# Kernel tuning notes

Measured on AMD Instinct MI355X. Metric: run time of the kernel, lower is better.

The kernel has to match this reference:

```python
import jax, jax.numpy as jnp
import numpy as np

B, C_IN, C_OUT, RED, H, W = 8, 256, 64, 16, 256, 256
K = 3


def setup_inputs() -> dict:
    key = jax.random.key(0)
    k1, k2, k3, k4, k5 = jax.random.split(key, 5)
    x = jax.random.normal(k1, (B, C_OUT, H, W), dtype=jnp.float32)
    vec = jax.random.normal(k2, (B, C_IN), dtype=jnp.float32)
    # ChanNorm affine params
    g = jnp.ones((1, C_OUT, 1, 1), dtype=jnp.float32)
    b = jnp.zeros((1, C_OUT, 1, 1), dtype=jnp.float32)
    # conv_du MLP (torch Linear weights: [out, in], no bias)
    w1 = jax.random.normal(k3, (C_IN // RED, C_IN), dtype=jnp.float32) / np.sqrt(C_IN)
    w2 = jax.random.normal(k4, (C_OUT, C_IN // RED), dtype=jnp.float32) / np.sqrt(C_IN // RED)
    # Conv2DMod weight, kaiming normal fan_in (leaky_relu a=0): std=sqrt(2/fan_in)
    fan_in = C_OUT * K * K
    wconv = jax.random.normal(k5, (C_OUT, C_OUT, K, K), dtype=jnp.float32) * np.sqrt(2.0 / fan_in)
    return {"x": x, "vec": vec, "g": g, "b": b, "w1": w1, "w2": w2, "wconv": wconv}


def reference(x, vec, g, b, w1, w2, wconv):
    eps_norm = 1e-5
    eps_mod = 1e-8
    # ChanNorm: normalize over channel dim (unbiased=False var)
    mean = jnp.mean(x, axis=1, keepdims=True)
    var = jnp.mean((x - mean) ** 2, axis=1, keepdims=True)
    nx = (x - mean) / jnp.sqrt(var + eps_norm) * g + b
    # style MLP: Linear -> LeakyReLU(0.1) -> Linear (no biases)
    hid = jax.nn.leaky_relu(vec @ w1.T, negative_slope=0.1)
    sty = hid @ w2.T  # [B, C_OUT]
    # per-sample modulated weights: [B, O, I, K, K]
    weights = wconv[None, :, :, :, :] * (sty[:, None, :, None, None] + 1.0)
    # demodulate
    d = jax.lax.rsqrt(jnp.sum(weights ** 2, axis=(2, 3, 4), keepdims=True) + eps_mod)
    weights = weights * d
    # grouped conv with groups=B == per-sample conv; same padding for k=3,s=1,d=1 -> 1
    pad = ((H - 1) * 0 + 1 * (K - 1)) // 2
    def per_sample_conv(xi, wi):
        # xi: [C,H,W], wi: [O,I,K,K]
        return jax.lax.conv_general_dilated(
            xi[None], wi, window_strides=(1, 1),
            padding=[(pad, pad), (pad, pad)],
            dimension_numbers=("NCHW", "OIHW", "NCHW"))[0]
    out = jax.vmap(per_sample_conv)(nx, weights)  # [B, O, H, W]
    return out + x
```

## Files before the change

### kernel.cpp

```cpp
#include <hip/hip_runtime.h>
#include <hip/hip_bf16.h>

typedef __hip_bfloat16 bf16;
typedef __attribute__((ext_vector_type(8))) short short8;
typedef __attribute__((ext_vector_type(4))) float float4v;

#define Hd 256
#define Wd 256
#define HW 65536
#define CO 64

__global__ __launch_bounds__(64) void k1_style(
    const float* __restrict__ vec, const float* __restrict__ w1,
    const float* __restrict__ w2, const float* __restrict__ wconv,
    bf16* __restrict__ wA)
{
    int o = blockIdx.x;
    int s = blockIdx.y;
    int i = threadIdx.x;

    float sv[4];
#pragma unroll
    for (int q = 0; q < 4; ++q) sv[q] = vec[s * 256 + q * 64 + i];

    float hid[16];
#pragma unroll
    for (int j = 0; j < 16; ++j) {
        float p = 0.f;
#pragma unroll
        for (int q = 0; q < 4; ++q) p += sv[q] * w1[j * 256 + q * 64 + i];
#pragma unroll
        for (int off = 32; off >= 1; off >>= 1) p += __shfl_xor(p, off, 64);
        hid[j] = p > 0.f ? p : 0.1f * p;
    }
    float sty = 0.f;
#pragma unroll
    for (int j = 0; j < 16; ++j) sty += w2[i * 16 + j] * hid[j];
    float msty = sty + 1.0f;

    float wrow[9];
#pragma unroll
    for (int tt = 0; tt < 9; ++tt) wrow[tt] = wconv[(o * 64 + i) * 9 + tt] * msty;
    float ss = 0.f;
#pragma unroll
    for (int tt = 0; tt < 9; ++tt) ss += wrow[tt] * wrow[tt];
#pragma unroll
    for (int off = 32; off >= 1; off >>= 1) ss += __shfl_xor(ss, off, 64);
    float d = rsqrtf(ss + 1e-8f);

    bf16* wAs = wA + s * (18 * 64 * 32);
#pragma unroll
    for (int tt = 0; tt < 9; ++tt) {
        int k = tt * 64 + i;
        wAs[(k >> 5) * 2048 + o * 32 + (k & 31)] = (bf16)(wrow[tt] * d);
    }
}

__global__ __launch_bounds__(256) void k2_norm(
    const float* __restrict__ x, const float* __restrict__ gg,
    const float* __restrict__ bb, bf16* __restrict__ nx,
    float2* __restrict__ sms)
{
    int bx  = blockIdx.x;
    int h   = bx >> 1;
    int seg = (bx & 1) * 128;
    int s   = blockIdx.y;
    int t   = threadIdx.x;
    int wave = t >> 6, lane = t & 63;
    int po = lane & 7;
    int cg = lane >> 3;

    __shared__ __align__(16) char lbuf[4][4096];

    int pxw = seg + wave * 32;
    const float* xrow = x + (size_t)s * ((size_t)CO * HW) + (size_t)h * Wd;

    float4 v[8];
#pragma unroll
    for (int c = 0; c < 8; ++c)
        v[c] = *(const float4*)&xrow[(size_t)(cg * 8 + c) * HW + pxw + po * 4];

    float s1[4], s2[4];
#pragma unroll
    for (int pi = 0; pi < 4; ++pi) {
        float a = 0.f, q = 0.f;
#pragma unroll
        for (int c = 0; c < 8; ++c) { float f = (&v[c].x)[pi]; a += f; q += f * f; }
        s1[pi] = a; s2[pi] = q;
    }
#pragma unroll
    for (int off = 8; off <= 32; off <<= 1)
#pragma unroll
        for (int pi = 0; pi < 4; ++pi) {
            s1[pi] += __shfl_xor(s1[pi], off, 64);
            s2[pi] += __shfl_xor(s2[pi], off, 64);
        }
    float mean[4], rstd[4];
#pragma unroll
    for (int pi = 0; pi < 4; ++pi) {
        mean[pi] = s1[pi] * (1.f / 64);
        float var = s2[pi] * (1.f / 64) - mean[pi] * mean[pi] + 1e-5f;
        rstd[pi] = rsqrtf(var);
    }
    if (cg == 0) {
        float2* smsrow = sms + (size_t)s * HW + (size_t)h * Wd;
#pragma unroll
        for (int pi = 0; pi < 4; ++pi) {
            float var = s2[pi] * (1.f / 64) - mean[pi] * mean[pi] + 1e-5f;
            smsrow[pxw + po * 4 + pi] = make_float2(mean[pi], var * rstd[pi]);
        }
    }

    float4 gA = *(const float4*)&gg[cg * 8], gB = *(const float4*)&gg[cg * 8 + 4];
    float4 bA = *(const float4*)&bb[cg * 8], bB = *(const float4*)&bb[cg * 8 + 4];
#pragma unroll
    for (int pi = 0; pi < 4; ++pi) {
        union { uint4 u; bf16 hh[8]; } ov;
#pragma unroll
        for (int c = 0; c < 8; ++c) {
            float gv = (c < 4) ? (&gA.x)[c] : (&gB.x)[c - 4];
            float bv = (c < 4) ? (&bA.x)[c] : (&bB.x)[c - 4];
            ov.hh[c] = (bf16)(((&v[c].x)[pi] - mean[pi]) * rstd[pi] * gv + bv);
        }
        int p = po * 4 + pi;
        *(uint4*)&lbuf[wave][(size_t)p * 128 + cg * 16] = ov.u;
    }
    __syncthreads();
    bf16* nxw = nx + ((size_t)s * HW + (size_t)h * Wd + pxw) * CO;
#pragma unroll
    for (int i = 0; i < 4; ++i) {
        uint4 d = *(uint4*)&lbuf[wave][i * 1024 + lane * 16];
        *(uint4*)((char*)nxw + i * 1024 + lane * 16) = d;
    }
}

#define PXB 32
#define ROWS 8
#define TR 10
#define WL 34
#define NSITES (TR * WL)
#define ROW_ELEMS (8 * WL * 8)

union U4 { uint4 u; bf16 h[8]; short8 s8; };

__global__ __launch_bounds__(256) void k3_conv(
    const bf16* __restrict__ nx, const float2* __restrict__ sms,
    const float* __restrict__ gg, const float* __restrict__ bb,
    const bf16* __restrict__ wA, float* __restrict__ out)
{
    int w0 = blockIdx.x * PXB;
    int h0 = blockIdx.y * ROWS;
    int s  = blockIdx.z;
    int t  = threadIdx.x;
    __shared__ __align__(16) bf16 tile[TR * ROW_ELEMS];
    __shared__ float2 sbi[64];
    if (t < 64) sbi[t] = make_float2(bb[t], 1.0f / gg[t]);

    int p0 = t, p1 = t + 256;
    bool live1 = (p1 < NSITES);
    int dr0 = p0 / WL, wl0 = p0 - dr0 * WL;
    int dr1 = live1 ? (p1 / WL) : 0;
    int wl1 = live1 ? (p1 - dr1 * WL) : 0;
    int grow0 = h0 + dr0 - 1, wab0 = w0 + wl0 - 1;
    int grow1 = h0 + dr1 - 1, wab1 = w0 + wl1 - 1;
    bool ok0 = (grow0 >= 0 && grow0 < Hd && wab0 >= 0 && wab0 < Wd);
    bool ok1 = live1 && (grow1 >= 0 && grow1 < Hd && wab1 >= 0 && wab1 < Wd);
    const bf16* np0 = nx + ((size_t)s * HW + (size_t)grow0 * Wd + wab0) * CO;
    const bf16* np1 = nx + ((size_t)s * HW + (size_t)grow1 * Wd + wab1) * CO;
    bf16* dst0 = &tile[dr0 * ROW_ELEMS + wl0 * 8];
    bf16* dst1 = &tile[dr1 * ROW_ELEMS + wl1 * 8];
    uint4 z = make_uint4(0u, 0u, 0u, 0u);
#pragma unroll
    for (int c8 = 0; c8 < 8; ++c8) {
        uint4 a = ok0 ? *(const uint4*)&np0[c8 * 8] : z;
        *(uint4*)&dst0[c8 * (WL * 8)] = a;
    }
    if (live1) {
#pragma unroll
        for (int c8 = 0; c8 < 8; ++c8) {
            uint4 a = ok1 ? *(const uint4*)&np1[c8 * 8] : z;
            *(uint4*)&dst1[c8 * (WL * 8)] = a;
        }
    }

    int wave = t >> 6, lane = t & 63;
    int mi = wave & 1, ni = wave >> 1;
    int col = lane & 15, quad = lane >> 4;

    const bf16* wAs = wA + s * (18 * 64 * 32);
    const bf16* pa0 = wAs + (mi * 32 + col) * 32 + quad * 8;
    const bf16* pa1 = wAs + (mi * 32 + 16 + col) * 32 + quad * 8;
    U4 a0c, a1c;
    a0c.u = *(const uint4*)pa0;
    a1c.u = *(const uint4*)pa1;

    int wpx = w0 + ni * 16 + col;
    float2 msr[ROWS];
#pragma unroll
    for (int r = 0; r < ROWS; ++r)
        msr[r] = sms[(size_t)s * HW + (size_t)(h0 + r) * Wd + wpx];

    __syncthreads();

    float2 bi8[2][4];
#pragma unroll
    for (int mt = 0; mt < 2; ++mt)
#pragma unroll
        for (int rr = 0; rr < 4; ++rr)
            bi8[mt][rr] = sbi[mi * 32 + mt * 16 + quad * 4 + rr];

    float4v acc[2][ROWS];
#pragma unroll
    for (int mt = 0; mt < 2; ++mt)
#pragma unroll
        for (int r = 0; r < ROWS; ++r) acc[mt][r] = (float4v)0.f;

    int base = ni * 16 + col;
#pragma unroll 1
    for (int kc = 0; kc < 18; ++kc) {
        U4 a0n, a1n;
        a0n.u = *(const uint4*)(pa0 + (kc + 1) * 2048);
        a1n.u = *(const uint4*)(pa1 + (kc + 1) * 2048);
        int tap = kc >> 1;
        int kh = (tap * 11) >> 5;
        int kw = tap - kh * 3;
        int ch8 = (kc & 1) * 4 + quad;
        const bf16* bp = &tile[kh * ROW_ELEMS + (ch8 * WL + base + kw) * 8];
#pragma unroll
        for (int r = 0; r < ROWS; ++r) {
            U4 b; b.u = *(const uint4*)&bp[r * ROW_ELEMS];
            acc[0][r] = __builtin_amdgcn_mfma_f32_16x16x32_bf16(a0c.s8, b.s8, acc[0][r], 0, 0, 0);
            acc[1][r] = __builtin_amdgcn_mfma_f32_16x16x32_bf16(a1c.s8, b.s8, acc[1][r], 0, 0, 0);
        }
        a0c = a0n; a1c = a1n;
    }

    int wl_i = base + 1;
#pragma unroll
    for (int r = 0; r < ROWS; ++r) {
        int grow = h0 + r;
        float2 ms = msr[r];
#pragma unroll
        for (int mt = 0; mt < 2; ++mt) {
            int o0 = mi * 32 + mt * 16 + quad * 4;
            int c8o = o0 >> 3;
            union { uint2 u; bf16 hh[4]; } nv;
            nv.u = *(const uint2*)&tile[(r + 1) * ROW_ELEMS + (c8o * WL + wl_i) * 8 + (o0 & 7)];
            size_t idx0 = (size_t)(s * CO + o0) * HW + (size_t)grow * Wd + wpx;
#pragma unroll
            for (int rr = 0; rr < 4; ++rr) {
                float2 bi = bi8[mt][rr];
                float xrec = (__bfloat162float(nv.hh[rr]) - bi.x) * bi.y * ms.y + ms.x;
                out[idx0 + (size_t)rr * HW] = acc[mt][r][rr] + xrec;
            }
        }
    }
}

extern "C" void kernel_launch(void* const* d_in, const int* in_sizes, int n_in,
                              void* d_out, int out_size, void* d_ws, size_t ws_size,
                              hipStream_t stream)
{
    const float* x     = (const float*)d_in[0];
    const float* vec   = (const float*)d_in[1];
    const float* g     = (const float*)d_in[2];
    const float* bb    = (const float*)d_in[3];
    const float* w1    = (const float*)d_in[4];
    const float* w2    = (const float*)d_in[5];
    const float* wconv = (const float*)d_in[6];
    float* out = (float*)d_out;

    char* wsb = (char*)d_ws;
    bf16*   wA  = (bf16*)wsb;
    bf16*   nx  = (bf16*)(wsb + ((size_t)1 << 20));
    float2* sms = (float2*)(wsb + ((size_t)65 << 20));

    k1_style<<<dim3(64, 8), 64, 0, stream>>>(vec, w1, w2, wconv, wA);
    k2_norm<<<dim3(512, 8), 256, 0, stream>>>(x, g, bb, nx, sms);
    k3_conv<<<dim3(8, 32, 8), 256, 0, stream>>>(nx, sms, g, bb, wA, out);
}
```

Baseline: 329.6 us.

## Widen norm blocks to full rows and restructure conv K-loop with preloaded weight fragments

```diff
diff --git a/kernel.cpp b/kernel.cpp
--- a/kernel.cpp
+++ b/kernel.cpp
@@ -61,35 +61,32 @@
     const float* __restrict__ bb, bf16* __restrict__ nx,
     float2* __restrict__ sms)
 {
-    int bx  = blockIdx.x;
-    int h   = bx >> 1;
-    int seg = (bx & 1) * 128;
-    int s   = blockIdx.y;
-    int t   = threadIdx.x;
+    int h = blockIdx.x, s = blockIdx.y;
+    int t = threadIdx.x;
     int wave = t >> 6, lane = t & 63;
-    int po = lane & 7;
-    int cg = lane >> 3;
-
-    __shared__ __align__(16) char lbuf[4][4096];
-
-    int pxw = seg + wave * 32;
+    int po = lane & 15;
+    int cg = lane >> 4;
+
+    __shared__ __align__(16) char lbuf[4][8192];
+
+    int pxw = wave * 64;
     const float* xrow = x + (size_t)s * ((size_t)CO * HW) + (size_t)h * Wd;
 
-    float4 v[8];
-#pragma unroll
-    for (int c = 0; c < 8; ++c)
-        v[c] = *(const float4*)&xrow[(size_t)(cg * 8 + c) * HW + pxw + po * 4];
+    float4 v[16];
+#pragma unroll
+    for (int c = 0; c < 16; ++c)
+        v[c] = *(const float4*)&xrow[(size_t)(cg * 16 + c) * HW + pxw + po * 4];
 
     float s1[4], s2[4];
 #pragma unroll
     for (int pi = 0; pi < 4; ++pi) {
         float a = 0.f, q = 0.f;
 #pragma unroll
-        for (int c = 0; c < 8; ++c) { float f = (&v[c].x)[pi]; a += f; q += f * f; }
+        for (int c = 0; c < 16; ++c) { float f = (&v[c].x)[pi]; a += f; q += f * f; }
         s1[pi] = a; s2[pi] = q;
     }
 #pragma unroll
-    for (int off = 8; off <= 32; off <<= 1)
+    for (int off = 16; off <= 32; off <<= 1)
 #pragma unroll
         for (int pi = 0; pi < 4; ++pi) {
             s1[pi] += __shfl_xor(s1[pi], off, 64);
@@ -107,30 +104,35 @@
 #pragma unroll
         for (int pi = 0; pi < 4; ++pi) {
             float var = s2[pi] * (1.f / 64) - mean[pi] * mean[pi] + 1e-5f;
-            smsrow[pxw + po * 4 + pi] = make_float2(mean[pi], var * rstd[pi]);
-        }
-    }
-
-    float4 gA = *(const float4*)&gg[cg * 8], gB = *(const float4*)&gg[cg * 8 + 4];
-    float4 bA = *(const float4*)&bb[cg * 8], bB = *(const float4*)&bb[cg * 8 + 4];
+            smsrow[pxw + po * 4 + pi] = make_float2(mean[pi], sqrtf(var));
+        }
+    }
+
+    float4 g4[4], b4[4];
+#pragma unroll
+    for (int j = 0; j < 4; ++j) {
+        g4[j] = *(const float4*)&gg[cg * 16 + j * 4];
+        b4[j] = *(const float4*)&bb[cg * 16 + j * 4];
+    }
 #pragma unroll
     for (int pi = 0; pi < 4; ++pi) {
-        union { uint4 u; bf16 hh[8]; } ov;
-#pragma unroll
-        for (int c = 0; c < 8; ++c) {
-            float gv = (c < 4) ? (&gA.x)[c] : (&gB.x)[c - 4];
-            float bv = (c < 4) ? (&bA.x)[c] : (&bB.x)[c - 4];
+        union { uint4 u[2]; bf16 hh[16]; } ov;
+#pragma unroll
+        for (int c = 0; c < 16; ++c) {
+            float gv = (&g4[c >> 2].x)[c & 3];
+            float bv = (&b4[c >> 2].x)[c & 3];
             ov.hh[c] = (bf16)(((&v[c].x)[pi] - mean[pi]) * rstd[pi] * gv + bv);
         }
         int p = po * 4 + pi;
-        *(uint4*)&lbuf[wave][(size_t)p * 128 + cg * 16] = ov.u;
+        *(uint4*)&lbuf[wave][(size_t)p * 128 + cg * 32] = ov.u[0];
+        *(uint4*)&lbuf[wave][(size_t)p * 128 + cg * 32 + 16] = ov.u[1];
     }
     __syncthreads();
-    bf16* nxw = nx + ((size_t)s * HW + (size_t)h * Wd + pxw) * CO;
-#pragma unroll
-    for (int i = 0; i < 4; ++i) {
+    char* nxw = (char*)(nx + ((size_t)s * HW + (size_t)h * Wd + pxw) * CO);
+#pragma unroll
+    for (int i = 0; i < 8; ++i) {
         uint4 d = *(uint4*)&lbuf[wave][i * 1024 + lane * 16];
-        *(uint4*)((char*)nxw + i * 1024 + lane * 16) = d;
+        *(uint4*)(nxw + i * 1024 + lane * 16) = d;
     }
 }
 
@@ -187,13 +189,6 @@
     int mi = wave & 1, ni = wave >> 1;
     int col = lane & 15, quad = lane >> 4;
 
-    const bf16* wAs = wA + s * (18 * 64 * 32);
-    const bf16* pa0 = wAs + (mi * 32 + col) * 32 + quad * 8;
-    const bf16* pa1 = wAs + (mi * 32 + 16 + col) * 32 + quad * 8;
-    U4 a0c, a1c;
-    a0c.u = *(const uint4*)pa0;
-    a1c.u = *(const uint4*)pa1;
-
     int wpx = w0 + ni * 16 + col;
     float2 msr[ROWS];
 #pragma unroll
@@ -202,37 +197,42 @@
 
     __syncthreads();
 
-    float2 bi8[2][4];
+    const bf16* wAs = wA + s * (18 * 64 * 32);
+    int a_off0 = (mi * 32 + col) * 32 + quad * 8;
+    int a_off1 = a_off0 + 16 * 32;
+    int base = ni * 16 + col;
+    const bf16* tbase = &tile[quad * 272 + base * 8];
+
+    float4v acc[2][ROWS];
 #pragma unroll
     for (int mt = 0; mt < 2; ++mt)
 #pragma unroll
-        for (int rr = 0; rr < 4; ++rr)
-            bi8[mt][rr] = sbi[mi * 32 + mt * 16 + quad * 4 + rr];
-
-    float4v acc[2][ROWS];
-#pragma unroll
-    for (int mt = 0; mt < 2; ++mt)
-#pragma unroll
         for (int r = 0; r < ROWS; ++r) acc[mt][r] = (float4v)0.f;
 
-    int base = ni * 16 + col;
 #pragma unroll 1
-    for (int kc = 0; kc < 18; ++kc) {
-        U4 a0n, a1n;
-        a0n.u = *(const uint4*)(pa0 + (kc + 1) * 2048);
-        a1n.u = *(const uint4*)(pa1 + (kc + 1) * 2048);
-        int tap = kc >> 1;
-        int kh = (tap * 11) >> 5;
-        int kw = tap - kh * 3;
-        int ch8 = (kc & 1) * 4 + quad;
-        const bf16* bp = &tile[kh * ROW_ELEMS + (ch8 * WL + base + kw) * 8];
+    for (int half = 0; half < 2; ++half) {
+        short8 af[9][2];
+#pragma unroll
+        for (int k9 = 0; k9 < 9; ++k9) {
+            U4 a0, a1;
+            a0.u = *(const uint4*)&wAs[(half * 9 + k9) * 2048 + a_off0];
+            a1.u = *(const uint4*)&wAs[(half * 9 + k9) * 2048 + a_off1];
+            af[k9][0] = a0.s8; af[k9][1] = a1.s8;
+        }
 #pragma unroll
         for (int r = 0; r < ROWS; ++r) {
-            U4 b; b.u = *(const uint4*)&bp[r * ROW_ELEMS];
-            acc[0][r] = __builtin_amdgcn_mfma_f32_16x16x32_bf16(a0c.s8, b.s8, acc[0][r], 0, 0, 0);
-            acc[1][r] = __builtin_amdgcn_mfma_f32_16x16x32_bf16(a1c.s8, b.s8, acc[1][r], 0, 0, 0);
-        }
-        a0c = a0n; a1c = a1n;
+            const bf16* rb = tbase + r * ROW_ELEMS;
+#pragma unroll
+            for (int k9 = 0; k9 < 9; ++k9) {
+                int kc = half * 9 + k9;
+                int tap = kc >> 1;
+                int kh = tap / 3, kw = tap - kh * 3;
+                U4 b;
+                b.u = *(const uint4*)&rb[kh * ROW_ELEMS + (kc & 1) * 1088 + kw * 8];
+                acc[0][r] = __builtin_amdgcn_mfma_f32_16x16x32_bf16(af[k9][0], b.s8, acc[0][r], 0, 0, 0);
+                acc[1][r] = __builtin_amdgcn_mfma_f32_16x16x32_bf16(af[k9][1], b.s8, acc[1][r], 0, 0, 0);
+            }
+        }
     }
 
     int wl_i = base + 1;
@@ -242,16 +242,15 @@
         float2 ms = msr[r];
 #pragma unroll
         for (int mt = 0; mt < 2; ++mt) {
-            int o0 = mi * 32 + mt * 16 + quad * 4;
-            int c8o = o0 >> 3;
-            union { uint2 u; bf16 hh[4]; } nv;
-            nv.u = *(const uint2*)&tile[(r + 1) * ROW_ELEMS + (c8o * WL + wl_i) * 8 + (o0 & 7)];
-            size_t idx0 = (size_t)(s * CO + o0) * HW + (size_t)grow * Wd + wpx;
 #pragma unroll
             for (int rr = 0; rr < 4; ++rr) {
-                float2 bi = bi8[mt][rr];
-                float xrec = (__bfloat162float(nv.hh[rr]) - bi.x) * bi.y * ms.y + ms.x;
-                out[idx0 + (size_t)rr * HW] = acc[mt][r][rr] + xrec;
+                int o = mi * 32 + mt * 16 + quad * 4 + rr;
+                float nxf = __bfloat162float(
+                    tile[(r + 1) * ROW_ELEMS + ((o >> 3) * WL + wl_i) * 8 + (o & 7)]);
+                float2 bi = sbi[o];
+                float xrec = (nxf - bi.x) * bi.y * ms.y + ms.x;
+                size_t idx = (size_t)(s * CO + o) * HW + (size_t)grow * Wd + wpx;
+                out[idx] = acc[mt][r][rr] + xrec;
             }
         }
     }
@@ -276,6 +275,6 @@
     float2* sms = (float2*)(wsb + ((size_t)65 << 20));
 
     k1_style<<<dim3(64, 8), 64, 0, stream>>>(vec, w1, w2, wconv, wA);
-    k2_norm<<<dim3(512, 8), 256, 0, stream>>>(x, g, bb, nx, sms);
+    k2_norm<<<dim3(256, 8), 256, 0, stream>>>(x, g, bb, nx, sms);
     k3_conv<<<dim3(8, 32, 8), 256, 0, stream>>>(nx, sms, g, bb, wA, out);
 }
```

Result: slower. 352.2 us (+6.8%).
